# Kernel optimization log

Hardware: AMD Instinct MI355X
Metric: run time of the kernel (lower is better)

## Reference

```python
import jax, jax.numpy as jnp
import numpy as np

NUM_CODE = 1024
DIM_CODE = 256
EPS = 1e-6


def setup_inputs() -> dict:
    key = jax.random.key(0)
    kz, ke = jax.random.split(key)
    z = jax.random.normal(kz, (32, 256, 32, 32), dtype=jnp.float32)
    # torch init: uniform(-1/num_code, 1/num_code)
    emb = jax.random.uniform(ke, (NUM_CODE, DIM_CODE), dtype=jnp.float32,
                             minval=-1.0 / NUM_CODE, maxval=1.0 / NUM_CODE)
    return {"z": z, "emb": emb}


def _l2norm(x, axis=-1):
    # F.normalize(p=2): x / max(||x||, eps_torch); torch default eps=1e-12
    n = jnp.sqrt(jnp.sum(x * x, axis=axis, keepdims=True))
    return x / jnp.maximum(n, 1e-12)


def reference(z, emb):
    N, C, H, W = z.shape
    z_flat = jnp.transpose(z, (0, 2, 3, 1)).reshape(N * H * W, C)  # (T, C)
    zn = _l2norm(z_flat, axis=1)
    en = _l2norm(emb, axis=1)
    # squared euclidean distance between normalized vectors
    d = (jnp.sum(zn * zn, axis=1, keepdims=True)
         + jnp.sum(en * en, axis=1)
         - 2.0 * jnp.matmul(zn, en.T))            # (T, K)
    min_idx = jnp.argmin(d, axis=1)               # (T,)
    quant = jnp.take(emb, min_idx, axis=0)        # (T, C) — gather of RAW codebook
    quant = jnp.transpose(quant.reshape(N, H, W, C), (0, 3, 1, 2))  # NCHW
    index = min_idx.reshape(N, H, W)
    return quant, index
```

## Files before the change

kernel.cpp:

```cpp
#include <hip/hip_runtime.h>

#define NTOK 32768
#define CDIM 256
#define KCODE 1024
#define C4 64

typedef __bf16 bf16x8 __attribute__((ext_vector_type(8)));
typedef float  f32x4  __attribute__((ext_vector_type(4)));
typedef const __attribute__((address_space(1))) void* as1cvp;
typedef __attribute__((address_space(3))) void* as3vp;

__device__ __forceinline__ unsigned long long umin64(unsigned long long a, unsigned long long b) { return a < b ? a : b; }
__device__ __forceinline__ unsigned long long umax64(unsigned long long a, unsigned long long b) { return a > b ? a : b; }

__global__ void k_prep(const float* __restrict__ z, const float* __restrict__ emb,
                       float* __restrict__ znt, float* __restrict__ znt2,
                       float* __restrict__ en, float* __restrict__ en2,
                       __bf16* __restrict__ eh, __bf16* __restrict__ el) {
    __shared__ float zsb[CDIM * 32];
    __shared__ float ssp[256];
    __shared__ float dens[32];
    int tid = threadIdx.x;

    if (blockIdx.x >= 1024) {
        int k = (blockIdx.x - 1024) * 64 + (tid >> 2);
        int q = tid & 3;
        const float4* ep = reinterpret_cast<const float4*>(emb) + (size_t)k * C4 + q * 16;
        float4 v[16];
        float ss = 0.f;
        #pragma unroll
        for (int i = 0; i < 16; ++i) {
            v[i] = ep[i];
            ss += v[i].x*v[i].x + v[i].y*v[i].y + v[i].z*v[i].z + v[i].w*v[i].w;
        }
        ss += __shfl_xor(ss, 1, 4); ss += __shfl_xor(ss, 2, 4);
        float den = fmaxf(sqrtf(ss), 1e-12f);
        float s2 = 0.f;
        float4* enp = reinterpret_cast<float4*>(en) + (size_t)k * C4 + q * 16;
        __bf16* ehp = eh + (size_t)k * CDIM + q * 64;
        __bf16* elp = el + (size_t)k * CDIM + q * 64;
        #pragma unroll
        for (int i = 0; i < 16; ++i) {
            float e4[4] = {v[i].x / den, v[i].y / den, v[i].z / den, v[i].w / den};
            enp[i] = make_float4(e4[0], e4[1], e4[2], e4[3]);
            #pragma unroll
            for (int j = 0; j < 4; ++j) {
                s2 += e4[j] * e4[j];
                __bf16 h = (__bf16)e4[j];
                ehp[i * 4 + j] = h;
                elp[i * 4 + j] = (__bf16)(e4[j] - (float)h);
            }
        }
        s2 += __shfl_xor(s2, 1, 4); s2 += __shfl_xor(s2, 2, 4);
        if (q == 0) en2[k] = s2;
        return;
    }

    int t0  = blockIdx.x * 32;
    int n   = t0 >> 10;
    int thw0 = t0 & 1023;

    int l = tid & 31, grp = tid >> 5;
    const float* zb = z + (((size_t)(n * CDIM)) << 10) + thw0 + l;
    float ss = 0.f;
    int c0 = grp * 32;
    for (int cc = 0; cc < 32; ++cc) {
        int c = c0 + cc;
        float v = zb[((size_t)c) << 10];
        zsb[c * 32 + ((l + c) & 31)] = v;
        ss += v * v;
    }
    ssp[tid] = ss;
    __syncthreads();
    if (tid < 32) {
        float tot = 0.f;
        #pragma unroll
        for (int g = 0; g < 8; ++g) tot += ssp[g * 32 + tid];
        dens[tid] = fmaxf(sqrtf(tot), 1e-12f);
    }
    __syncthreads();

    int l2 = tid & 63, tg = tid >> 6;
    for (int it = 0; it < 8; ++it) {
        int tok = tg * 8 + it;
        float den = dens[tok];
        float s2 = 0.f;
        #pragma unroll
        for (int cq = 0; cq < 4; ++cq) {
            int c = cq * 64 + l2;
            float v = zsb[c * 32 + ((tok + c) & 31)] / den;
            znt[((size_t)(t0 + tok)) * CDIM + c] = v;
            s2 += v * v;
        }
        #pragma unroll
        for (int o = 32; o >= 1; o >>= 1) s2 += __shfl_xor(s2, o, 64);
        if (l2 == 0) znt2[t0 + tok] = s2;
    }
}

__global__ __launch_bounds__(256, 2) void k_mfma(
        const float* __restrict__ znt,
        const __bf16* __restrict__ eh, const __bf16* __restrict__ el,
        const float* __restrict__ en2g,
        const float* __restrict__ znt2, const float* __restrict__ en,
        const float* __restrict__ emb, float* __restrict__ out) {
    __shared__ __align__(16) char smem_u[69632];
    __shared__ unsigned long long t2l[64][2][2];
    __shared__ int idxs[64];
    __bf16* ebuf = reinterpret_cast<__bf16*>(smem_u);
    float*  en2s = reinterpret_cast<float*>(smem_u + 65536);
    float*  qt   = reinterpret_cast<float*>(smem_u);

    int tid = threadIdx.x;
    int l = tid & 63, wid = tid >> 6;
    int mw = wid >> 1, nw = wid & 1;
    int t0 = blockIdx.x * 64;
    int row = l & 15, kg = l >> 4;

    for (int i = tid; i < KCODE; i += 256) en2s[i] = en2g[i];

    bf16x8 ah[2][8], al_[2][8];
    #pragma unroll
    for (int mt = 0; mt < 2; ++mt) {
        size_t tok = (size_t)(t0 + mw * 32 + mt * 16 + row);
        const float* pz = znt + tok * CDIM + kg * 8;
        #pragma unroll
        for (int ks = 0; ks < 8; ++ks) {
            float f[8];
            *reinterpret_cast<float4*>(&f[0]) = *reinterpret_cast<const float4*>(pz + ks * 32);
            *reinterpret_cast<float4*>(&f[4]) = *reinterpret_cast<const float4*>(pz + ks * 32 + 4);
            bf16x8 h, lo;
            #pragma unroll
            for (int q = 0; q < 8; ++q) {
                __bf16 hv = (__bf16)f[q];
                h[q] = hv;
                lo[q] = (__bf16)(f[q] - (float)hv);
            }
            ah[mt][ks] = h; al_[mt][ks] = lo;
        }
    }

    unsigned long long b1[8], b2[8];
    #pragma unroll
    for (int i = 0; i < 8; ++i) { b1[i] = ~0ull; b2[i] = ~0ull; }

    auto stage = [&](int buf, int ch) {
        #pragma unroll
        for (int a = 0; a < 2; ++a) {
            const __bf16* src = a ? el : eh;
            #pragma unroll
            for (int i2 = 0; i2 < 4; ++i2) {
                int s = i2 * 256 + tid;
                int code = s >> 5, c16 = s & 31;
                int gslot = c16 ^ (code & 15);
                const __bf16* gp = src + ((size_t)(ch * 32 + code)) * CDIM + gslot * 8;
                __bf16* ld = ebuf + (size_t)(buf * 2 + a) * 8192 + (size_t)(i2 * 256 + wid * 64) * 8;
                __builtin_amdgcn_global_load_lds((as1cvp)gp, (as3vp)ld, 16, 0, 0);
            }
        }
    };

    stage(0, 0);
    __syncthreads();
    #pragma unroll 2
    for (int ch = 0; ch < 32; ++ch) {
        int cur = ch & 1;
        if (ch < 31) stage(cur ^ 1, ch + 1);

        const __bf16* bh_base = ebuf + (size_t)(cur * 2 + 0) * 8192;
        const __bf16* bl_base = ebuf + (size_t)(cur * 2 + 1) * 8192;

        f32x4 a0[2], a1[2], a2[2];
        #pragma unroll
        for (int mt = 0; mt < 2; ++mt)
            #pragma unroll
            for (int r = 0; r < 4; ++r) { a0[mt][r] = 0.f; a1[mt][r] = 0.f; a2[mt][r] = 0.f; }

        int code_l = nw * 16 + row;
        #pragma unroll
        for (int ks = 0; ks < 8; ++ks) {
            int slot = (ks * 4 + kg) ^ row;
            bf16x8 bh = *reinterpret_cast<const bf16x8*>(bh_base + code_l * 256 + slot * 8);
            bf16x8 bl = *reinterpret_cast<const bf16x8*>(bl_base + code_l * 256 + slot * 8);
            #pragma unroll
            for (int mt = 0; mt < 2; ++mt) {
                a0[mt] = __builtin_amdgcn_mfma_f32_16x16x32_bf16(ah[mt][ks],  bh, a0[mt], 0, 0, 0);
                a1[mt] = __builtin_amdgcn_mfma_f32_16x16x32_bf16(ah[mt][ks],  bl, a1[mt], 0, 0, 0);
                a2[mt] = __builtin_amdgcn_mfma_f32_16x16x32_bf16(al_[mt][ks], bh, a2[mt], 0, 0, 0);
            }
        }

        int code = ch * 32 + code_l;
        float e2v = en2s[code];
        #pragma unroll
        for (int mt = 0; mt < 2; ++mt)
            #pragma unroll
            for (int r = 0; r < 4; ++r) {
                float d = fmaf(-2.0f, (a0[mt][r] + a1[mt][r]) + a2[mt][r], e2v);
                unsigned ub = __float_as_uint(d);
                ub = (ub & 0x80000000u) ? ~ub : (ub | 0x80000000u);
                unsigned long long key = ((unsigned long long)ub << 32) | (unsigned)code;
                int idx = mt * 4 + r;
                if (key < b1[idx]) { b2[idx] = b1[idx]; b1[idx] = key; }
                else if (key < b2[idx]) { b2[idx] = key; }
            }
        __syncthreads();
    }

    #pragma unroll
    for (int i = 0; i < 8; ++i) {
        #pragma unroll
        for (int off = 1; off < 16; off <<= 1) {
            unsigned long long o1 = __shfl_xor(b1[i], off, 16);
            unsigned long long o2 = __shfl_xor(b2[i], off, 16);
            unsigned long long m1 = umin64(b1[i], o1);
            unsigned long long m2 = umin64(umax64(b1[i], o1), umin64(b2[i], o2));
            b1[i] = m1; b2[i] = m2;
        }
    }
    if ((l & 15) == 0) {
        #pragma unroll
        for (int mt = 0; mt < 2; ++mt)
            #pragma unroll
            for (int r = 0; r < 4; ++r) {
                int tl = mw * 32 + mt * 16 + kg * 4 + r;
                t2l[tl][nw][0] = b1[mt * 4 + r];
                t2l[tl][nw][1] = b2[mt * 4 + r];
            }
    }
    __syncthreads();

    {
        int tl = tid >> 2, q = tid & 3;
        int t = t0 + tl;
        unsigned long long x1 = t2l[tl][0][0], x2 = t2l[tl][0][1];
        unsigned long long y1 = t2l[tl][1][0], y2 = t2l[tl][1][1];
        unsigned c1 = (unsigned)umin64(x1, y1);
        unsigned c2 = (unsigned)umin64(umax64(x1, y1), umin64(x2, y2));
        const float4* zp  = reinterpret_cast<const float4*>(znt) + (size_t)t  * C4 + q * 16;
        const float4* eap = reinterpret_cast<const float4*>(en)  + (size_t)c1 * C4 + q * 16;
        const float4* ebp = reinterpret_cast<const float4*>(en)  + (size_t)c2 * C4 + q * 16;
        float da = 0.f, db = 0.f;
        #pragma unroll
        for (int i = 0; i < 16; ++i) {
            float4 zv = zp[i], av = eap[i], bv = ebp[i];
            da += zv.x*av.x + zv.y*av.y + zv.z*av.z + zv.w*av.w;
            db += zv.x*bv.x + zv.y*bv.y + zv.z*bv.z + zv.w*bv.w;
        }
        da += __shfl_xor(da, 1, 4); da += __shfl_xor(da, 2, 4);
        db += __shfl_xor(db, 1, 4); db += __shfl_xor(db, 2, 4);
        if (q == 0) {
            float z2 = znt2[t];
            float d1 = (z2 + en2s[c1]) - 2.0f * da;
            float d2 = (z2 + en2s[c2]) - 2.0f * db;
            int k = (d2 < d1 || (d2 == d1 && c2 < c1)) ? (int)c2 : (int)c1;
            idxs[tl] = k;
            out[(size_t)NTOK * CDIM + t] = (float)k;
        }
    }
    __syncthreads();

    {
        int tl = tid & 63, q = tid >> 6;
        int kidx = idxs[tl];
        const float4* ep = reinterpret_cast<const float4*>(emb + (size_t)kidx * CDIM + q * 64);
        #pragma unroll
        for (int i = 0; i < 16; ++i) {
            float4 v = ep[i];
            int cb = q * 64 + i * 4;
            qt[tl * 257 + cb + 0] = v.x;
            qt[tl * 257 + cb + 1] = v.y;
            qt[tl * 257 + cb + 2] = v.z;
            qt[tl * 257 + cb + 3] = v.w;
        }
    }
    __syncthreads();

    {
        int hwo = tid & 63, cg = tid >> 6;
        int n = t0 >> 10, hw = (t0 & 1023) + hwo;
        float* ob = out + (size_t)n * (CDIM * 1024) + hw;
        #pragma unroll 8
        for (int cc = 0; cc < 64; ++cc) {
            int c = cg * 64 + cc;
            ob[(size_t)c * 1024] = qt[hwo * 257 + c];
        }
    }
}

extern "C" void kernel_launch(void* const* d_in, const int* in_sizes, int n_in,
                              void* d_out, int out_size, void* d_ws, size_t ws_size,
                              hipStream_t stream) {
    const float* z   = (const float*)d_in[0];
    const float* emb = (const float*)d_in[1];
    float* out  = (float*)d_out;

    float*  en   = (float*)d_ws;
    float*  en2  = en + (size_t)KCODE * CDIM;
    float*  znt2 = en2 + KCODE;
    __bf16* eh   = (__bf16*)(znt2 + NTOK);
    __bf16* el   = eh + (size_t)KCODE * CDIM;
    float*  znt  = (float*)(el + (size_t)KCODE * CDIM);

    k_prep<<<1024 + 16, 256, 0, stream>>>(z, emb, znt, znt2, en, en2, eh, el);
    k_mfma<<<NTOK / 64, 256, 0, stream>>>(znt, eh, el, en2, znt2, en, emb, out);
}
```

Measured before the change: 102.1 us.

## Software-pipeline argmin epilogue of previous chunk with current chunk MFMAs

```diff
diff --git a/kernel.cpp b/kernel.cpp
--- a/kernel.cpp
+++ b/kernel.cpp
@@ -160,51 +160,77 @@
         }
     };
 
-    stage(0, 0);
-    __syncthreads();
-    #pragma unroll 2
-    for (int ch = 0; ch < 32; ++ch) {
-        int cur = ch & 1;
-        if (ch < 31) stage(cur ^ 1, ch + 1);
-
+    struct Acc { f32x4 v[2][3]; };
+    Acc accA, accB;
+
+    int code_l = nw * 16 + row;
+
+    auto body = [&](int ch, int cur, Acc& acc, Acc& accP, int chP,
+                    bool doEpi, bool doStage) {
+        if (doStage) stage(cur ^ 1, ch + 1);
         const __bf16* bh_base = ebuf + (size_t)(cur * 2 + 0) * 8192;
         const __bf16* bl_base = ebuf + (size_t)(cur * 2 + 1) * 8192;
-
-        f32x4 a0[2], a1[2], a2[2];
         #pragma unroll
         for (int mt = 0; mt < 2; ++mt)
             #pragma unroll
-            for (int r = 0; r < 4; ++r) { a0[mt][r] = 0.f; a1[mt][r] = 0.f; a2[mt][r] = 0.f; }
-
-        int code_l = nw * 16 + row;
+            for (int tm = 0; tm < 3; ++tm)
+                #pragma unroll
+                for (int r = 0; r < 4; ++r) acc.v[mt][tm][r] = 0.f;
+
+        int codeP = chP * 32 + code_l;
+        float e2vP = doEpi ? en2s[codeP] : 0.f;
+
         #pragma unroll
         for (int ks = 0; ks < 8; ++ks) {
             int slot = (ks * 4 + kg) ^ row;
             bf16x8 bh = *reinterpret_cast<const bf16x8*>(bh_base + code_l * 256 + slot * 8);
             bf16x8 bl = *reinterpret_cast<const bf16x8*>(bl_base + code_l * 256 + slot * 8);
-            #pragma unroll
-            for (int mt = 0; mt < 2; ++mt) {
-                a0[mt] = __builtin_amdgcn_mfma_f32_16x16x32_bf16(ah[mt][ks],  bh, a0[mt], 0, 0, 0);
-                a1[mt] = __builtin_amdgcn_mfma_f32_16x16x32_bf16(ah[mt][ks],  bl, a1[mt], 0, 0, 0);
-                a2[mt] = __builtin_amdgcn_mfma_f32_16x16x32_bf16(al_[mt][ks], bh, a2[mt], 0, 0, 0);
-            }
-        }
-
-        int code = ch * 32 + code_l;
-        float e2v = en2s[code];
-        #pragma unroll
-        for (int mt = 0; mt < 2; ++mt)
-            #pragma unroll
-            for (int r = 0; r < 4; ++r) {
-                float d = fmaf(-2.0f, (a0[mt][r] + a1[mt][r]) + a2[mt][r], e2v);
+            acc.v[0][0] = __builtin_amdgcn_mfma_f32_16x16x32_bf16(ah[0][ks],  bh, acc.v[0][0], 0, 0, 0);
+            acc.v[0][1] = __builtin_amdgcn_mfma_f32_16x16x32_bf16(ah[0][ks],  bl, acc.v[0][1], 0, 0, 0);
+            acc.v[0][2] = __builtin_amdgcn_mfma_f32_16x16x32_bf16(al_[0][ks], bh, acc.v[0][2], 0, 0, 0);
+            acc.v[1][0] = __builtin_amdgcn_mfma_f32_16x16x32_bf16(ah[1][ks],  bh, acc.v[1][0], 0, 0, 0);
+            acc.v[1][1] = __builtin_amdgcn_mfma_f32_16x16x32_bf16(ah[1][ks],  bl, acc.v[1][1], 0, 0, 0);
+            acc.v[1][2] = __builtin_amdgcn_mfma_f32_16x16x32_bf16(al_[1][ks], bh, acc.v[1][2], 0, 0, 0);
+            if (doEpi) {
+                int mt = ks >> 2, r = ks & 3;
+                float d = fmaf(-2.0f, (accP.v[mt][0][r] + accP.v[mt][1][r]) + accP.v[mt][2][r], e2vP);
                 unsigned ub = __float_as_uint(d);
                 ub = (ub & 0x80000000u) ? ~ub : (ub | 0x80000000u);
-                unsigned long long key = ((unsigned long long)ub << 32) | (unsigned)code;
+                unsigned long long key = ((unsigned long long)ub << 32) | (unsigned)codeP;
                 int idx = mt * 4 + r;
                 if (key < b1[idx]) { b2[idx] = b1[idx]; b1[idx] = key; }
                 else if (key < b2[idx]) { b2[idx] = key; }
             }
+        }
+    };
+
+    stage(0, 0);
+    __syncthreads();
+    body(0, 0, accA, accB, 0, false, true);
+    __syncthreads();
+    #pragma unroll 1
+    for (int i = 0; i < 15; ++i) {
+        body(2 * i + 1, 1, accB, accA, 2 * i,     true, true);
         __syncthreads();
+        body(2 * i + 2, 0, accA, accB, 2 * i + 1, true, true);
+        __syncthreads();
+    }
+    body(31, 1, accB, accA, 30, true, false);
+
+    {
+        int code = 31 * 32 + code_l;
+        float e2v = en2s[code];
+        #pragma unroll
+        for (int p = 0; p < 8; ++p) {
+            int mt = p >> 2, r = p & 3;
+            float d = fmaf(-2.0f, (accB.v[mt][0][r] + accB.v[mt][1][r]) + accB.v[mt][2][r], e2v);
+            unsigned ub = __float_as_uint(d);
+            ub = (ub & 0x80000000u) ? ~ub : (ub | 0x80000000u);
+            unsigned long long key = ((unsigned long long)ub << 32) | (unsigned)code;
+            int idx = mt * 4 + r;
+            if (key < b1[idx]) { b2[idx] = b1[idx]; b1[idx] = key; }
+            else if (key < b2[idx]) { b2[idx] = key; }
+        }
     }
 
     #pragma unroll
```

Result: slower. 156.9 us (+53.7%).
